# Performance work log

Hardware: AMD Instinct MI355X
Metric: run time of the kernel (lower is better)

The kernel has to match this reference:

```python
import jax, jax.numpy as jnp
import numpy as np

N, E, D, H, C, K = 50000, 800000, 64, 16, 40, 2


def setup_inputs() -> dict:
    key = jax.random.key(0)
    ks = jax.random.split(key, 6)
    x = jax.random.normal(ks[0], (N, D), dtype=jnp.float32)
    edge_index = jax.random.randint(ks[1], (2, E), 0, N, dtype=jnp.int32)
    W1 = jax.random.normal(ks[2], (K, D, H), dtype=jnp.float32) * 0.1
    b1 = jax.random.normal(ks[3], (H,), dtype=jnp.float32) * 0.1
    W2 = jax.random.normal(ks[4], (K, H, C), dtype=jnp.float32) * 0.1
    b2 = jax.random.normal(ks[5], (C,), dtype=jnp.float32) * 0.1
    return {"x": x, "edge_index": edge_index, "W1": W1, "b1": b1, "W2": W2, "b2": b2}


def _cheb_conv(x, src, dst, norm, W, b):
    # PyG ChebConv, K=2, sym norm, lambda_max=2:
    # scaled Laplacian L_hat = -D^{-1/2} A D^{-1/2}  (diag cancels to 0)
    # out = Tx0 @ W[0] + Tx1 @ W[1] + b,  Tx0 = x,  Tx1 = L_hat x
    n = x.shape[0]
    msgs = norm[:, None] * x[src]                      # [E, F] gather
    Tx1 = jax.ops.segment_sum(msgs, dst, num_segments=n)  # scatter-add
    return x @ W[0] + Tx1 @ W[1] + b


def reference(x, edge_index, W1, b1, W2, b2):
    src, dst = edge_index[0], edge_index[1]
    n = x.shape[0]
    # symmetric normalization coefficients (edge weights = 1)
    deg = jax.ops.segment_sum(jnp.ones((src.shape[0],), x.dtype), src, num_segments=n)
    dinv = jnp.where(deg > 0, jax.lax.rsqrt(jnp.maximum(deg, 1.0)), 0.0)
    norm = -dinv[src] * dinv[dst]
    h = jax.nn.relu(_cheb_conv(x, src, dst, norm, W1, b1))
    # dropout is identity in eval mode
    out = _cheb_conv(h, src, dst, norm, W2, b2)
    return jax.nn.log_softmax(out, axis=1)
```

## Files before the change

kernel.cpp:

```cpp
#include <hip/hip_runtime.h>
#include <math.h>

#define N_NODES 50000
#define N_EDGES 800000
#define D_IN    64
#define H_HID   16
#define C_OUT   40

#define BSH     7
#define BNODES  128
#define BMASK   127
#define NBUCK   ((N_NODES + BNODES - 1) / BNODES)
#define NBUCKP  400
#define NBLK    500
#define EPB     (N_EDGES / NBLK)
#define EPB4    (EPB / 4)

__global__ void bucket_count(const int* __restrict__ src, const int* __restrict__ dst,
                             int* __restrict__ partS, int* __restrict__ partD) {
    __shared__ int hS[NBUCK], hD[NBUCK];
    for (int i = threadIdx.x; i < NBUCK; i += blockDim.x) { hS[i] = 0; hD[i] = 0; }
    __syncthreads();
    const int4* s4 = (const int4*)(src + blockIdx.x * EPB);
    const int4* d4 = (const int4*)(dst + blockIdx.x * EPB);
    for (int k = threadIdx.x; k < EPB4; k += blockDim.x) {
        int4 s = s4[k], d = d4[k];
        atomicAdd(&hS[s.x >> BSH], 1); atomicAdd(&hS[s.y >> BSH], 1);
        atomicAdd(&hS[s.z >> BSH], 1); atomicAdd(&hS[s.w >> BSH], 1);
        atomicAdd(&hD[d.x >> BSH], 1); atomicAdd(&hD[d.y >> BSH], 1);
        atomicAdd(&hD[d.z >> BSH], 1); atomicAdd(&hD[d.w >> BSH], 1);
    }
    __syncthreads();
    for (int i = threadIdx.x; i < NBUCK; i += blockDim.x) {
        partS[blockIdx.x * NBUCKP + i] = hS[i];
        partD[blockIdx.x * NBUCKP + i] = hD[i];
    }
}

__global__ void bucket_base_scan(int* __restrict__ partS, int* __restrict__ partD,
                                 int* __restrict__ totS, int* __restrict__ totD) {
    int* part = blockIdx.y ? partD : partS;
    int* tot  = blockIdx.y ? totD  : totS;
    int b = blockIdx.x;
    __shared__ int s[512];
    int k = threadIdx.x;
    int v = (k < NBLK) ? part[k * NBUCKP + b] : 0;
    s[k] = v;
    __syncthreads();
    for (int off = 1; off < 512; off <<= 1) {
        int t = (k >= off) ? s[k - off] : 0;
        __syncthreads();
        s[k] += t;
        __syncthreads();
    }
    if (k < NBLK) part[k * NBUCKP + b] = s[k] - v;
    if (k == 511) tot[b] = s[511];
}

__global__ void bucket_base_final(const int* __restrict__ totS, const int* __restrict__ totD,
                                  int* __restrict__ baseS, int* __restrict__ baseD) {
    const int* tot = blockIdx.x ? totD : totS;
    int* base = blockIdx.x ? baseD : baseS;
    __shared__ int s[512];
    int k = threadIdx.x;
    int v = (k < NBUCK) ? tot[k] : 0;
    s[k] = v;
    __syncthreads();
    for (int off = 1; off < 512; off <<= 1) {
        int t = (k >= off) ? s[k - off] : 0;
        __syncthreads();
        s[k] += t;
        __syncthreads();
    }
    if (k < NBUCK) base[k] = s[k] - v;
    if (k == NBUCK - 1) base[NBUCK] = s[k];
}

__global__ void bucket_scatter(const int* __restrict__ src, const int* __restrict__ dst,
                               const int* __restrict__ partS, const int* __restrict__ partD,
                               const int* __restrict__ baseS, const int* __restrict__ baseD,
                               unsigned int* __restrict__ packedD,
                               unsigned char* __restrict__ srcloc) {
    __shared__ int cS[NBUCK], cD[NBUCK];
    int blk = blockIdx.x;
    for (int b = threadIdx.x; b < NBUCK; b += blockDim.x) {
        cS[b] = baseS[b] + partS[blk * NBUCKP + b];
        cD[b] = baseD[b] + partD[blk * NBUCKP + b];
    }
    __syncthreads();
    const int4* s4 = (const int4*)(src + blk * EPB);
    const int4* d4 = (const int4*)(dst + blk * EPB);
    for (int k = threadIdx.x; k < EPB4; k += blockDim.x) {
        int4 sv = s4[k], dv = d4[k];
        int ss[4] = { sv.x, sv.y, sv.z, sv.w };
        int dd[4] = { dv.x, dv.y, dv.z, dv.w };
        #pragma unroll
        for (int u = 0; u < 4; ++u) {
            int s = ss[u], d = dd[u];
            int pD = atomicAdd(&cD[d >> BSH], 1);
            packedD[pD] = (unsigned)s | ((unsigned)(d & BMASK) << 16);
            int pS = atomicAdd(&cS[s >> BSH], 1);
            srcloc[pS] = (unsigned char)(s & BMASK);
        }
    }
}

__global__ void csr_build(const unsigned int* __restrict__ packedD, const int* __restrict__ baseD,
                          const unsigned char* __restrict__ srcloc, const int* __restrict__ baseS,
                          int* __restrict__ col, int* __restrict__ rowptr,
                          float* __restrict__ dinv) {
    __shared__ int hist[BNODES], scanv[BNODES], cur[BNODES], shist[BNODES];
    int tid = threadIdx.x;
    if (tid < BNODES) { hist[tid] = 0; shist[tid] = 0; }
    __syncthreads();
    int bb = blockIdx.x;
    int begD = baseD[bb], endD = baseD[bb + 1];
    for (int j = begD + tid; j < endD; j += blockDim.x)
        atomicAdd(&hist[(packedD[j] >> 16) & BMASK], 1);
    int begS = baseS[bb], endS = baseS[bb + 1];
    for (int j = begS + tid; j < endS; j += blockDim.x)
        atomicAdd(&shist[srcloc[j]], 1);
    __syncthreads();
    if (tid == 0) {
        int acc = 0;
        for (int i = 0; i < BNODES; ++i) { scanv[i] = acc; acc += hist[i]; }
    }
    __syncthreads();
    if (tid < BNODES) {
        cur[tid] = scanv[tid];
        int node = bb * BNODES + tid;
        if (node < N_NODES) {
            rowptr[node] = begD + scanv[tid];
            int d = shist[tid];
            dinv[node] = (d > 0) ? rsqrtf((float)d) : 0.0f;
        }
    }
    if (bb == NBUCK - 1 && tid == 0) rowptr[N_NODES] = endD;
    __syncthreads();
    for (int j = begD + tid; j < endD; j += blockDim.x) {
        unsigned rec = packedD[j];
        int dl = (rec >> 16) & BMASK;
        int pos = atomicAdd(&cur[dl], 1);
        col[begD + pos] = (int)(rec & 0xFFFF);
    }
}

__global__ void xw_kernel(const float* __restrict__ x, const float* __restrict__ W1,
                          const float* __restrict__ dinv,
                          float* __restrict__ xw0, float* __restrict__ sxw1) {
    __shared__ float sW[2 * D_IN * H_HID];
    __shared__ float sx[16 * 65];
    for (int i = threadIdx.x; i < 2 * D_IN * H_HID; i += 256) sW[i] = W1[i];
    int nbase = blockIdx.x * 16;
    for (int i = threadIdx.x; i < 16 * D_IN; i += 256) {
        int r = i >> 6, c = i & 63;
        sx[r * 65 + c] = x[(size_t)(nbase + r) * D_IN + c];
    }
    __syncthreads();
    int nl = threadIdx.x >> 4, f = threadIdx.x & 15;
    int node = nbase + nl;
    float a0 = 0.f, a1 = 0.f;
    #pragma unroll
    for (int d = 0; d < D_IN; ++d) {
        float xv = sx[nl * 65 + d];
        a0 += xv * sW[d * H_HID + f];
        a1 += xv * sW[D_IN * H_HID + d * H_HID + f];
    }
    int t = node * H_HID + f;
    xw0[t]  = a0;
    sxw1[t] = dinv[node] * a1;
}

#define GATHER16(TBL)                                                              \
    for (; j + 16 <= end; j += 16) {                                               \
        int cc[16];                                                                \
        _Pragma("unroll")                                                          \
        for (int u = 0; u < 16; ++u) cc[u] = col[j + u];                           \
        float4 vv[16];                                                             \
        _Pragma("unroll")                                                          \
        for (int u = 0; u < 16; ++u) vv[u] = TBL[cc[u] * 4 + f4];                  \
        _Pragma("unroll")                                                          \
        for (int u = 0; u < 16; ++u) {                                             \
            a.x += vv[u].x; a.y += vv[u].y; a.z += vv[u].z; a.w += vv[u].w;        \
        }                                                                          \
    }                                                                              \
    for (; j + 8 <= end; j += 8) {                                                 \
        int cc[8];                                                                 \
        _Pragma("unroll")                                                          \
        for (int u = 0; u < 8; ++u) cc[u] = col[j + u];                            \
        float4 vv[8];                                                              \
        _Pragma("unroll")                                                          \
        for (int u = 0; u < 8; ++u) vv[u] = TBL[cc[u] * 4 + f4];                   \
        _Pragma("unroll")                                                          \
        for (int u = 0; u < 8; ++u) {                                              \
            a.x += vv[u].x; a.y += vv[u].y; a.z += vv[u].z; a.w += vv[u].w;        \
        }                                                                          \
    }                                                                              \
    for (; j < end; ++j) {                                                         \
        float4 v = TBL[col[j] * 4 + f4];                                           \
        a.x += v.x; a.y += v.y; a.z += v.z; a.w += v.w;                            \
    }

__global__ void gather1(const int* __restrict__ rowptr, const int* __restrict__ col,
                        const float* __restrict__ dinv, const float* __restrict__ sxw1,
                        const float* __restrict__ xw0, const float* __restrict__ b1,
                        float* __restrict__ h, float* __restrict__ sh) {
    int grp = threadIdx.x >> 2;
    int f4  = threadIdx.x & 3;
    int node = blockIdx.x * 128 + grp;
    if (node >= N_NODES) return;
    int beg = rowptr[node], end = rowptr[node + 1];
    const float4* sx4 = (const float4*)sxw1;
    float4 a = make_float4(0.f, 0.f, 0.f, 0.f);
    int j = beg;
    GATHER16(sx4)
    float di = dinv[node];
    float4 x0 = ((const float4*)xw0)[node * 4 + f4];
    float4 bb = ((const float4*)b1)[f4];
    float vx = fmaxf(x0.x - di * a.x + bb.x, 0.f);
    float vy = fmaxf(x0.y - di * a.y + bb.y, 0.f);
    float vz = fmaxf(x0.z - di * a.z + bb.z, 0.f);
    float vw = fmaxf(x0.w - di * a.w + bb.w, 0.f);
    ((float4*)h)[node * 4 + f4]  = make_float4(vx, vy, vz, vw);
    ((float4*)sh)[node * 4 + f4] = make_float4(di * vx, di * vy, di * vz, di * vw);
}

#define HROW 20
__global__ void gather2_out(const int* __restrict__ rowptr, const int* __restrict__ col,
                            const float* __restrict__ dinv, const float* __restrict__ sh,
                            const float* __restrict__ h, const float* __restrict__ W2,
                            const float* __restrict__ b2, float* __restrict__ out) {
    __shared__ float sW0[H_HID * C_OUT], sW1[H_HID * C_OUT], sb[C_OUT];
    __shared__ float hrow[128][HROW];
    __shared__ float trow[128][HROW];
    for (int i = threadIdx.x; i < H_HID * C_OUT; i += 512) {
        sW0[i] = W2[i];
        sW1[i] = W2[H_HID * C_OUT + i];
    }
    if (threadIdx.x < C_OUT) sb[threadIdx.x] = b2[threadIdx.x];

    int grp = threadIdx.x >> 2;
    int f4  = threadIdx.x & 3;
    int node = blockIdx.x * 128 + grp;
    bool active = node < N_NODES;
    int beg = 0, end = 0;
    float di = 0.f;
    if (active) { beg = rowptr[node]; end = rowptr[node + 1]; di = dinv[node]; }
    const float4* sh4 = (const float4*)sh;
    float4 a = make_float4(0.f, 0.f, 0.f, 0.f);
    int j = beg;
    GATHER16(sh4)
    float4 hp = make_float4(0.f, 0.f, 0.f, 0.f);
    if (active) hp = ((const float4*)h)[node * 4 + f4];
    hrow[grp][4 * f4 + 0] = hp.x;
    hrow[grp][4 * f4 + 1] = hp.y;
    hrow[grp][4 * f4 + 2] = hp.z;
    hrow[grp][4 * f4 + 3] = hp.w;
    trow[grp][4 * f4 + 0] = -di * a.x;
    trow[grp][4 * f4 + 1] = -di * a.y;
    trow[grp][4 * f4 + 2] = -di * a.z;
    trow[grp][4 * f4 + 3] = -di * a.w;
    __syncthreads();

    float hv[H_HID], tv[H_HID];
    #pragma unroll
    for (int ff = 0; ff < H_HID; ++ff) {
        hv[ff] = hrow[grp][ff];
        tv[ff] = trow[grp][ff];
    }
    float o[10];
    float mx = -1e30f;
    #pragma unroll
    for (int i = 0; i < 10; ++i) {
        int c = f4 * 10 + i;
        float aa = sb[c];
        #pragma unroll
        for (int ff = 0; ff < H_HID; ++ff)
            aa += hv[ff] * sW0[ff * C_OUT + c] + tv[ff] * sW1[ff * C_OUT + c];
        o[i] = aa;
        mx = fmaxf(mx, aa);
    }
    mx = fmaxf(mx, __shfl_xor(mx, 1));
    mx = fmaxf(mx, __shfl_xor(mx, 2));
    float sum = 0.f;
    #pragma unroll
    for (int i = 0; i < 10; ++i) sum += expf(o[i] - mx);
    sum += __shfl_xor(sum, 1);
    sum += __shfl_xor(sum, 2);
    float lse = mx + logf(sum);
    if (active) {
        float* op = out + (size_t)node * C_OUT + f4 * 10;
        #pragma unroll
        for (int i = 0; i < 10; ++i) op[i] = o[i] - lse;
    }
}

extern "C" void kernel_launch(void* const* d_in, const int* in_sizes, int n_in,
                              void* d_out, int out_size, void* d_ws, size_t ws_size,
                              hipStream_t stream) {
    const float* x   = (const float*)d_in[0];
    const int*   ei  = (const int*)d_in[1];
    const float* W1  = (const float*)d_in[2];
    const float* b1  = (const float*)d_in[3];
    const float* W2  = (const float*)d_in[4];
    const float* b2  = (const float*)d_in[5];
    float* out = (float*)d_out;

    const int* src = ei;
    const int* dst = ei + N_EDGES;

    int* partS = (int*)d_ws;
    int* partD = partS + NBLK * NBUCKP;
    int* baseS = partD + NBLK * NBUCKP;
    int* baseD = baseS + 512;
    int* totS  = baseD + 512;
    int* totD  = totS + 512;
    unsigned int*  packedD = (unsigned int*)(totD + 512);
    unsigned char* srcloc  = (unsigned char*)(packedD + N_EDGES);
    int*   col    = (int*)(srcloc + N_EDGES);
    int*   rowptr = col + N_EDGES;
    float* dinv   = (float*)(rowptr + N_NODES + 8);
    float* xw0    = dinv + N_NODES;
    float* sxw1   = xw0  + (size_t)N_NODES * H_HID;
    float* h      = sxw1 + (size_t)N_NODES * H_HID;
    float* sh     = h    + (size_t)N_NODES * H_HID;

    bucket_count     <<<NBLK, 256, 0, stream>>>(src, dst, partS, partD);
    bucket_base_scan <<<dim3(NBUCK, 2), 512, 0, stream>>>(partS, partD, totS, totD);
    bucket_base_final<<<2, 512, 0, stream>>>(totS, totD, baseS, baseD);
    bucket_scatter   <<<NBLK, 256, 0, stream>>>(src, dst, partS, partD, baseS, baseD, packedD, srcloc);
    csr_build        <<<NBUCK, 512, 0, stream>>>(packedD, baseD, srcloc, baseS, col, rowptr, dinv);
    xw_kernel        <<<N_NODES / 16, 256, 0, stream>>>(x, W1, dinv, xw0, sxw1);
    gather1          <<<(N_NODES + 127) / 128, 512, 0, stream>>>(rowptr, col, dinv, sxw1, xw0, b1, h, sh);
    gather2_out      <<<(N_NODES + 127) / 128, 512, 0, stream>>>(rowptr, col, dinv, sh, h, W2, b2, out);
}
```

Before: 90.31 us.

## Store gather tables in fp16 and column indices as 16-bit to cut gather traffic

The per-node feature tables read in the two neighbour-gather kernels (sxw1, h, sh) are now stored as half precision, and the CSR column array is stored as unsigned short instead of int. Each gathered row segment becomes 8 bytes instead of 16, and each index 2 bytes instead of 4, roughly halving the random-access traffic that dominates the gathers. Block size for both gather kernels drops from 512 to 256 threads (64 nodes per block). The cost is fp16 rounding of intermediate activations, which may loosen accuracy against the fp32 reference.

```diff
diff --git a/kernel.cpp b/kernel.cpp
--- a/kernel.cpp
+++ b/kernel.cpp
@@ -1,4 +1,5 @@
 #include <hip/hip_runtime.h>
+#include <hip/hip_fp16.h>
 #include <math.h>
 
 #define N_NODES 50000
@@ -107,7 +108,7 @@
 
 __global__ void csr_build(const unsigned int* __restrict__ packedD, const int* __restrict__ baseD,
                           const unsigned char* __restrict__ srcloc, const int* __restrict__ baseS,
-                          int* __restrict__ col, int* __restrict__ rowptr,
+                          unsigned short* __restrict__ col, int* __restrict__ rowptr,
                           float* __restrict__ dinv) {
     __shared__ int hist[BNODES], scanv[BNODES], cur[BNODES], shist[BNODES];
     int tid = threadIdx.x;
@@ -141,13 +142,13 @@
         unsigned rec = packedD[j];
         int dl = (rec >> 16) & BMASK;
         int pos = atomicAdd(&cur[dl], 1);
-        col[begD + pos] = (int)(rec & 0xFFFF);
+        col[begD + pos] = (unsigned short)(rec & 0xFFFF);
     }
 }
 
 __global__ void xw_kernel(const float* __restrict__ x, const float* __restrict__ W1,
                           const float* __restrict__ dinv,
-                          float* __restrict__ xw0, float* __restrict__ sxw1) {
+                          float* __restrict__ xw0, __half* __restrict__ sxw1h) {
     __shared__ float sW[2 * D_IN * H_HID];
     __shared__ float sx[16 * 65];
     for (int i = threadIdx.x; i < 2 * D_IN * H_HID; i += 256) sW[i] = W1[i];
@@ -167,73 +168,81 @@
         a1 += xv * sW[D_IN * H_HID + d * H_HID + f];
     }
     int t = node * H_HID + f;
-    xw0[t]  = a0;
-    sxw1[t] = dinv[node] * a1;
-}
-
-#define GATHER16(TBL)                                                              \
-    for (; j + 16 <= end; j += 16) {                                               \
-        int cc[16];                                                                \
-        _Pragma("unroll")                                                          \
-        for (int u = 0; u < 16; ++u) cc[u] = col[j + u];                           \
-        float4 vv[16];                                                             \
-        _Pragma("unroll")                                                          \
-        for (int u = 0; u < 16; ++u) vv[u] = TBL[cc[u] * 4 + f4];                  \
-        _Pragma("unroll")                                                          \
-        for (int u = 0; u < 16; ++u) {                                             \
-            a.x += vv[u].x; a.y += vv[u].y; a.z += vv[u].z; a.w += vv[u].w;        \
-        }                                                                          \
-    }                                                                              \
-    for (; j + 8 <= end; j += 8) {                                                 \
-        int cc[8];                                                                 \
-        _Pragma("unroll")                                                          \
-        for (int u = 0; u < 8; ++u) cc[u] = col[j + u];                            \
-        float4 vv[8];                                                              \
-        _Pragma("unroll")                                                          \
-        for (int u = 0; u < 8; ++u) vv[u] = TBL[cc[u] * 4 + f4];                   \
-        _Pragma("unroll")                                                          \
-        for (int u = 0; u < 8; ++u) {                                              \
-            a.x += vv[u].x; a.y += vv[u].y; a.z += vv[u].z; a.w += vv[u].w;        \
-        }                                                                          \
-    }                                                                              \
-    for (; j < end; ++j) {                                                         \
-        float4 v = TBL[col[j] * 4 + f4];                                           \
-        a.x += v.x; a.y += v.y; a.z += v.z; a.w += v.w;                            \
-    }
-
-__global__ void gather1(const int* __restrict__ rowptr, const int* __restrict__ col,
-                        const float* __restrict__ dinv, const float* __restrict__ sxw1,
+    xw0[t]   = a0;
+    sxw1h[t] = __float2half_rn(dinv[node] * a1);
+}
+
+#define ACC4(V)                                                       \
+    {                                                                 \
+        __half2 p0 = *reinterpret_cast<const __half2*>(&(V).x);       \
+        __half2 p1 = *reinterpret_cast<const __half2*>(&(V).y);       \
+        float2 f0 = __half22float2(p0), f1 = __half22float2(p1);      \
+        a0 += f0.x; a1 += f0.y; a2 += f1.x; a3 += f1.y;               \
+    }
+
+#define GATHERH(TBL)                                                  \
+    for (; j + 16 <= end; j += 16) {                                  \
+        int cc[16];                                                   \
+        _Pragma("unroll")                                             \
+        for (int u = 0; u < 16; ++u) cc[u] = col[j + u];              \
+        uint2 vv[16];                                                 \
+        _Pragma("unroll")                                             \
+        for (int u = 0; u < 16; ++u) vv[u] = TBL[cc[u] * 4 + f4];     \
+        _Pragma("unroll")                                             \
+        for (int u = 0; u < 16; ++u) ACC4(vv[u])                      \
+    }                                                                 \
+    for (; j + 8 <= end; j += 8) {                                    \
+        int cc[8];                                                    \
+        _Pragma("unroll")                                             \
+        for (int u = 0; u < 8; ++u) cc[u] = col[j + u];               \
+        uint2 vv[8];                                                  \
+        _Pragma("unroll")                                             \
+        for (int u = 0; u < 8; ++u) vv[u] = TBL[cc[u] * 4 + f4];      \
+        _Pragma("unroll")                                             \
+        for (int u = 0; u < 8; ++u) ACC4(vv[u])                       \
+    }                                                                 \
+    for (; j < end; ++j) {                                            \
+        uint2 v = TBL[col[j] * 4 + f4];                               \
+        ACC4(v)                                                       \
+    }
+
+__global__ void gather1(const int* __restrict__ rowptr, const unsigned short* __restrict__ col,
+                        const float* __restrict__ dinv, const uint2* __restrict__ sxw1h,
                         const float* __restrict__ xw0, const float* __restrict__ b1,
-                        float* __restrict__ h, float* __restrict__ sh) {
+                        uint2* __restrict__ h16, uint2* __restrict__ sh16) {
     int grp = threadIdx.x >> 2;
     int f4  = threadIdx.x & 3;
-    int node = blockIdx.x * 128 + grp;
+    int node = blockIdx.x * 64 + grp;
     if (node >= N_NODES) return;
     int beg = rowptr[node], end = rowptr[node + 1];
-    const float4* sx4 = (const float4*)sxw1;
-    float4 a = make_float4(0.f, 0.f, 0.f, 0.f);
+    float a0 = 0.f, a1 = 0.f, a2 = 0.f, a3 = 0.f;
     int j = beg;
-    GATHER16(sx4)
+    GATHERH(sxw1h)
     float di = dinv[node];
     float4 x0 = ((const float4*)xw0)[node * 4 + f4];
     float4 bb = ((const float4*)b1)[f4];
-    float vx = fmaxf(x0.x - di * a.x + bb.x, 0.f);
-    float vy = fmaxf(x0.y - di * a.y + bb.y, 0.f);
-    float vz = fmaxf(x0.z - di * a.z + bb.z, 0.f);
-    float vw = fmaxf(x0.w - di * a.w + bb.w, 0.f);
-    ((float4*)h)[node * 4 + f4]  = make_float4(vx, vy, vz, vw);
-    ((float4*)sh)[node * 4 + f4] = make_float4(di * vx, di * vy, di * vz, di * vw);
+    float v0 = fmaxf(x0.x - di * a0 + bb.x, 0.f);
+    float v1 = fmaxf(x0.y - di * a1 + bb.y, 0.f);
+    float v2 = fmaxf(x0.z - di * a2 + bb.z, 0.f);
+    float v3 = fmaxf(x0.w - di * a3 + bb.w, 0.f);
+    uint2 hw, sw;
+    *reinterpret_cast<__half2*>(&hw.x) = __float22half2_rn(make_float2(v0, v1));
+    *reinterpret_cast<__half2*>(&hw.y) = __float22half2_rn(make_float2(v2, v3));
+    *reinterpret_cast<__half2*>(&sw.x) = __float22half2_rn(make_float2(di * v0, di * v1));
+    *reinterpret_cast<__half2*>(&sw.y) = __float22half2_rn(make_float2(di * v2, di * v3));
+    h16[node * 4 + f4]  = hw;
+    sh16[node * 4 + f4] = sw;
 }
 
 #define HROW 20
-__global__ void gather2_out(const int* __restrict__ rowptr, const int* __restrict__ col,
-                            const float* __restrict__ dinv, const float* __restrict__ sh,
-                            const float* __restrict__ h, const float* __restrict__ W2,
+__global__ void gather2_out(const int* __restrict__ rowptr, const unsigned short* __restrict__ col,
+                            const float* __restrict__ dinv, const uint2* __restrict__ sh16,
+                            const uint2* __restrict__ h16, const float* __restrict__ W2,
                             const float* __restrict__ b2, float* __restrict__ out) {
     __shared__ float sW0[H_HID * C_OUT], sW1[H_HID * C_OUT], sb[C_OUT];
-    __shared__ float hrow[128][HROW];
-    __shared__ float trow[128][HROW];
-    for (int i = threadIdx.x; i < H_HID * C_OUT; i += 512) {
+    __shared__ float hrow[64][HROW];
+    __shared__ float trow[64][HROW];
+    for (int i = threadIdx.x; i < H_HID * C_OUT; i += 256) {
         sW0[i] = W2[i];
         sW1[i] = W2[H_HID * C_OUT + i];
     }
@@ -241,25 +250,30 @@
 
     int grp = threadIdx.x >> 2;
     int f4  = threadIdx.x & 3;
-    int node = blockIdx.x * 128 + grp;
+    int node = blockIdx.x * 64 + grp;
     bool active = node < N_NODES;
     int beg = 0, end = 0;
     float di = 0.f;
     if (active) { beg = rowptr[node]; end = rowptr[node + 1]; di = dinv[node]; }
-    const float4* sh4 = (const float4*)sh;
-    float4 a = make_float4(0.f, 0.f, 0.f, 0.f);
+    float a0 = 0.f, a1 = 0.f, a2 = 0.f, a3 = 0.f;
     int j = beg;
-    GATHER16(sh4)
-    float4 hp = make_float4(0.f, 0.f, 0.f, 0.f);
-    if (active) hp = ((const float4*)h)[node * 4 + f4];
-    hrow[grp][4 * f4 + 0] = hp.x;
-    hrow[grp][4 * f4 + 1] = hp.y;
-    hrow[grp][4 * f4 + 2] = hp.z;
-    hrow[grp][4 * f4 + 3] = hp.w;
-    trow[grp][4 * f4 + 0] = -di * a.x;
-    trow[grp][4 * f4 + 1] = -di * a.y;
-    trow[grp][4 * f4 + 2] = -di * a.z;
-    trow[grp][4 * f4 + 3] = -di * a.w;
+    GATHERH(sh16)
+    float h0 = 0.f, h1 = 0.f, h2 = 0.f, h3 = 0.f;
+    if (active) {
+        uint2 hv2 = h16[node * 4 + f4];
+        __half2 p0 = *reinterpret_cast<const __half2*>(&hv2.x);
+        __half2 p1 = *reinterpret_cast<const __half2*>(&hv2.y);
+        float2 f0 = __half22float2(p0), f1 = __half22float2(p1);
+        h0 = f0.x; h1 = f0.y; h2 = f1.x; h3 = f1.y;
+    }
+    hrow[grp][4 * f4 + 0] = h0;
+    hrow[grp][4 * f4 + 1] = h1;
+    hrow[grp][4 * f4 + 2] = h2;
+    hrow[grp][4 * f4 + 3] = h3;
+    trow[grp][4 * f4 + 0] = -di * a0;
+    trow[grp][4 * f4 + 1] = -di * a1;
+    trow[grp][4 * f4 + 2] = -di * a2;
+    trow[grp][4 * f4 + 3] = -di * a3;
     __syncthreads();
 
     float hv[H_HID], tv[H_HID];
@@ -315,22 +329,24 @@
     int* baseD = baseS + 512;
     int* totS  = baseD + 512;
     int* totD  = totS + 512;
-    unsigned int*  packedD = (unsigned int*)(totD + 512);
-    unsigned char* srcloc  = (unsigned char*)(packedD + N_EDGES);
-    int*   col    = (int*)(srcloc + N_EDGES);
-    int*   rowptr = col + N_EDGES;
+    unsigned int*   packedD = (unsigned int*)(totD + 512);
+    unsigned char*  srcloc  = (unsigned char*)(packedD + N_EDGES);
+    unsigned short* col     = (unsigned short*)(srcloc + N_EDGES);
+    int*   rowptr = (int*)(col + N_EDGES);
     float* dinv   = (float*)(rowptr + N_NODES + 8);
     float* xw0    = dinv + N_NODES;
-    float* sxw1   = xw0  + (size_t)N_NODES * H_HID;
-    float* h      = sxw1 + (size_t)N_NODES * H_HID;
-    float* sh     = h    + (size_t)N_NODES * H_HID;
+    __half* sxw1h = (__half*)(xw0 + (size_t)N_NODES * H_HID);
+    __half* h16   = sxw1h + (size_t)N_NODES * H_HID;
+    __half* sh16  = h16   + (size_t)N_NODES * H_HID;
 
     bucket_count     <<<NBLK, 256, 0, stream>>>(src, dst, partS, partD);
     bucket_base_scan <<<dim3(NBUCK, 2), 512, 0, stream>>>(partS, partD, totS, totD);
     bucket_base_final<<<2, 512, 0, stream>>>(totS, totD, baseS, baseD);
     bucket_scatter   <<<NBLK, 256, 0, stream>>>(src, dst, partS, partD, baseS, baseD, packedD, srcloc);
     csr_build        <<<NBUCK, 512, 0, stream>>>(packedD, baseD, srcloc, baseS, col, rowptr, dinv);
-    xw_kernel        <<<N_NODES / 16, 256, 0, stream>>>(x, W1, dinv, xw0, sxw1);
-    gather1          <<<(N_NODES + 127) / 128, 512, 0, stream>>>(rowptr, col, dinv, sxw1, xw0, b1, h, sh);
-    gather2_out      <<<(N_NODES + 127) / 128, 512, 0, stream>>>(rowptr, col, dinv, sh, h, W2, b2, out);
-}
+    xw_kernel        <<<N_NODES / 16, 256, 0, stream>>>(x, W1, dinv, xw0, sxw1h);
+    gather1          <<<(N_NODES + 63) / 64, 256, 0, stream>>>(rowptr, col, dinv, (const uint2*)sxw1h,
+                                                               xw0, b1, (uint2*)h16, (uint2*)sh16);
+    gather2_out      <<<(N_NODES + 63) / 64, 256, 0, stream>>>(rowptr, col, dinv, (const uint2*)sh16,
+                                                               (const uint2*)h16, W2, b2, out);
+}
```

Result: faster. 82.56 us (median of 2 runs) (-8.6%).
